# Kernel optimization log

Hardware: AMD Instinct MI355X
Metric: run time of the kernel (lower is better)

## Reference

```python
import jax, jax.numpy as jnp
import numpy as np

N = 50000      # nodes
E = 800000     # edges
IN = 128       # in_feats
HID = 16       # h_feats (per head)
HEADS = 8      # num_heads layer 1
CLS = 40       # num_classes
NEG_SLOPE = 0.2


def setup_inputs() -> dict:
    key = jax.random.key(0)
    ks = jax.random.split(key, 12)
    s = lambda fan: np.float32(1.0 / np.sqrt(fan))
    return {
        "features": jax.random.normal(ks[0], (N, IN), jnp.float32),
        "edge_src": jax.random.randint(ks[1], (E,), 0, N, dtype=jnp.int32),
        "edge_dst": jax.random.randint(ks[2], (E,), 0, N, dtype=jnp.int32),
        # layer 1 params
        "W1": jax.random.normal(ks[3], (IN, HEADS * HID), jnp.float32) * s(IN),
        "al1": jax.random.normal(ks[4], (HEADS, HID), jnp.float32) * s(HID),
        "ar1": jax.random.normal(ks[5], (HEADS, HID), jnp.float32) * s(HID),
        "b1": jnp.zeros((HEADS * HID,), jnp.float32),
        # layer 2 params (1 head)
        "W2": jax.random.normal(ks[6], (HEADS * HID, CLS), jnp.float32) * s(HEADS * HID),
        "al2": jax.random.normal(ks[7], (1, CLS), jnp.float32) * s(CLS),
        "ar2": jax.random.normal(ks[8], (1, CLS), jnp.float32) * s(CLS),
        "b2": jnp.zeros((CLS,), jnp.float32),
    }


def gat_conv(x, W, al, ar, b, src, dst, heads, out_dim):
    # x: [N, F_in] -> feat: [N, H, D]
    feat = (x @ W).reshape(-1, heads, out_dim)
    el = (feat * al).sum(-1)                      # [N, H]
    er = (feat * ar).sum(-1)                      # [N, H]
    e = jax.nn.leaky_relu(el[src] + er[dst], NEG_SLOPE)  # [E, H]
    # segment softmax over destination neighborhoods
    emax = jax.ops.segment_max(e, dst, num_segments=N)   # [N, H]
    emax = jnp.where(jnp.isfinite(emax), emax, jnp.float32(0.0))
    ee = jnp.exp(e - emax[dst])                   # [E, H]
    denom = jax.ops.segment_sum(ee, dst, num_segments=N)
    alpha = ee / (denom[dst] + jnp.float32(1e-9)) # [E, H]
    msg = alpha[:, :, None] * feat[src]           # [E, H, D]
    out = jax.ops.segment_sum(msg, dst, num_segments=N)  # [N, H, D]
    return out + b.reshape(1, heads, out_dim)


def reference(features, edge_src, edge_dst, W1, al1, ar1, b1, W2, al2, ar2, b2):
    h = jax.nn.elu(gat_conv(features, W1, al1, ar1, b1, edge_src, edge_dst, HEADS, HID))
    h = h.reshape(N, HEADS * HID)                 # flatten(1)
    out = gat_conv(h, W2, al2, ar2, b2, edge_src, edge_dst, 1, CLS)
    return out.mean(axis=1)                       # [N, CLS]
```

## Files before the change

### kernel.cpp

```cpp
#include <hip/hip_runtime.h>
#include <hip/hip_bf16.h>

#define N_NODES 50000
#define N_EDGES 800000
#define IN_F    128
#define HID     16
#define HEADS   8
#define F1      128
#define CLS     40
#define CLSP    64
#define NEG     0.2f
#define NEG_INF (-__builtin_inff())
#define SWEEPS      8
#define SWEEP_RANGE 6250
#define STRIDE      96

typedef __bf16 bf16x8 __attribute__((ext_vector_type(8)));
typedef float  f32x4  __attribute__((ext_vector_type(4)));
typedef float  f32x2  __attribute__((ext_vector_type(2)));

__device__ __forceinline__ float leaky(float v) { return v >= 0.0f ? v : NEG * v; }
__device__ __forceinline__ f32x2 unpk(unsigned u) {
    f32x2 r;
    r.x = __uint_as_float(u << 16);
    r.y = __uint_as_float(u & 0xffff0000u);
    return r;
}

__global__ void setup_kernel(const float* __restrict__ W1, const float* __restrict__ W2,
                             __bf16* __restrict__ w1t, __bf16* __restrict__ w2t,
                             int* __restrict__ cursor) {
    int i = blockIdx.x * blockDim.x + threadIdx.x;
    if (i < N_NODES) cursor[i] = 0;
    if (i < 128 * 128) {
        int n = i >> 7, k = i & 127;
        w1t[i] = (__bf16)W1[k * 128 + n];
    }
    if (i < CLSP * 128) {
        int n = i >> 7, k = i & 127;
        w2t[i] = (n < CLS) ? (__bf16)W2[k * CLS + n] : (__bf16)0.0f;
    }
}

__global__ void scatter_kernel(const int* __restrict__ src, const int* __restrict__ dst,
                               int* __restrict__ cursor, int* __restrict__ srcs_sorted) {
    const int BPS = (N_EDGES + 255) / 256;
    int sweep = blockIdx.x / BPS;
    int e = (blockIdx.x - sweep * BPS) * 256 + threadIdx.x;
    if (e >= N_EDGES) return;
    int d = dst[e];
    int lo = sweep * SWEEP_RANGE;
    if (d < lo || d >= lo + SWEEP_RANGE) return;
    int pos = d * STRIDE + atomicAdd(&cursor[d], 1);
    srcs_sorted[pos] = src[e];
}

__global__ __launch_bounds__(256) void gemm1_mfma(const float* __restrict__ A,
                                                  const __bf16* __restrict__ Wt,
                                                  const float* __restrict__ al1,
                                                  const float* __restrict__ ar1,
                                                  __bf16* __restrict__ outb,
                                                  float* __restrict__ el,
                                                  float* __restrict__ er) {
    int wave = threadIdx.x >> 6, lane = threadIdx.x & 63;
    int m0 = blockIdx.x * 64 + wave * 16;
    int c = lane & 15;
    int row = m0 + c;
    int rowc = row < N_NODES ? row : N_NODES - 1;
    int ko = (lane >> 4) * 8;

    f32x4 acc[8];
    #pragma unroll
    for (int t = 0; t < 8; ++t)
        #pragma unroll
        for (int r = 0; r < 4; ++r) acc[t][r] = 0.f;

    for (int ks = 0; ks < 128; ks += 32) {
        const float* ap = A + (size_t)rowc * 128 + ks + ko;
        float4 u = *(const float4*)ap;
        float4 v = *(const float4*)(ap + 4);
        bf16x8 a;
        a[0] = (__bf16)u.x; a[1] = (__bf16)u.y; a[2] = (__bf16)u.z; a[3] = (__bf16)u.w;
        a[4] = (__bf16)v.x; a[5] = (__bf16)v.y; a[6] = (__bf16)v.z; a[7] = (__bf16)v.w;
        #pragma unroll
        for (int t = 0; t < 8; ++t) {
            bf16x8 b = *(const bf16x8*)(Wt + (size_t)(t * 16 + c) * 128 + ks + ko);
            acc[t] = __builtin_amdgcn_mfma_f32_16x16x32_bf16(a, b, acc[t], 0, 0, 0);
        }
    }
    int rbase = m0 + (lane >> 4) * 4;
    #pragma unroll
    for (int t = 0; t < 8; ++t) {
        int gcol = t * 16 + c;
        #pragma unroll
        for (int r = 0; r < 4; ++r) {
            int grow = rbase + r;
            if (grow < N_NODES) outb[(size_t)grow * 128 + gcol] = (__bf16)acc[t][r];
        }
    }
    #pragma unroll
    for (int t = 0; t < 8; ++t) {
        float alv = al1[t * 16 + c];
        float arv = ar1[t * 16 + c];
        float pe[4], pr[4];
        #pragma unroll
        for (int r = 0; r < 4; ++r) { pe[r] = acc[t][r] * alv; pr[r] = acc[t][r] * arv; }
        #pragma unroll
        for (int mask = 1; mask <= 8; mask <<= 1) {
            #pragma unroll
            for (int r = 0; r < 4; ++r) {
                pe[r] += __shfl_xor(pe[r], mask, 64);
                pr[r] += __shfl_xor(pr[r], mask, 64);
            }
        }
        if (c == 0) {
            #pragma unroll
            for (int r = 0; r < 4; ++r) {
                int grow = rbase + r;
                if (grow < N_NODES) {
                    el[grow * 8 + t] = pe[r];
                    er[grow * 8 + t] = pr[r];
                }
            }
        }
    }
}

__global__ __launch_bounds__(256) void gemm2_mfma(const __bf16* __restrict__ A,
                                                  const __bf16* __restrict__ Wt,
                                                  const float* __restrict__ al2,
                                                  const float* __restrict__ ar2,
                                                  __bf16* __restrict__ out,
                                                  float* __restrict__ el,
                                                  float* __restrict__ er) {
    int wave = threadIdx.x >> 6, lane = threadIdx.x & 63;
    int m0 = blockIdx.x * 64 + wave * 16;
    int c = lane & 15;
    int row = m0 + c;
    int rowc = row < N_NODES ? row : N_NODES - 1;
    int ko = (lane >> 4) * 8;

    f32x4 acc[4];
    #pragma unroll
    for (int t = 0; t < 4; ++t)
        #pragma unroll
        for (int r = 0; r < 4; ++r) acc[t][r] = 0.f;

    for (int ks = 0; ks < 128; ks += 32) {
        bf16x8 a = *(const bf16x8*)(A + (size_t)rowc * 128 + ks + ko);
        #pragma unroll
        for (int t = 0; t < 4; ++t) {
            bf16x8 b = *(const bf16x8*)(Wt + (size_t)(t * 16 + c) * 128 + ks + ko);
            acc[t] = __builtin_amdgcn_mfma_f32_16x16x32_bf16(a, b, acc[t], 0, 0, 0);
        }
    }
    int rbase = m0 + (lane >> 4) * 4;
    #pragma unroll
    for (int t = 0; t < 4; ++t) {
        int gcol = t * 16 + c;
        #pragma unroll
        for (int r = 0; r < 4; ++r) {
            int grow = rbase + r;
            if (grow < N_NODES) out[(size_t)grow * CLSP + gcol] = (__bf16)acc[t][r];
        }
    }
    float pe[4] = {0.f, 0.f, 0.f, 0.f}, pr[4] = {0.f, 0.f, 0.f, 0.f};
    #pragma unroll
    for (int t = 0; t < 3; ++t) {
        int idx = t * 16 + c;
        float alv = (idx < CLS) ? al2[idx] : 0.f;
        float arv = (idx < CLS) ? ar2[idx] : 0.f;
        #pragma unroll
        for (int r = 0; r < 4; ++r) { pe[r] += acc[t][r] * alv; pr[r] += acc[t][r] * arv; }
    }
    #pragma unroll
    for (int mask = 1; mask <= 8; mask <<= 1) {
        #pragma unroll
        for (int r = 0; r < 4; ++r) {
            pe[r] += __shfl_xor(pe[r], mask, 64);
            pr[r] += __shfl_xor(pr[r], mask, 64);
        }
    }
    if (c == 0) {
        #pragma unroll
        for (int r = 0; r < 4; ++r) {
            int grow = rbase + r;
            if (grow < N_NODES) { el[grow] = pe[r]; er[grow] = pr[r]; }
        }
    }
}

__global__ __launch_bounds__(256) void gat1_fused(const int* __restrict__ degs,
                                                  const int* __restrict__ srcs,
                                                  const float* __restrict__ el,
                                                  const float* __restrict__ er,
                                                  const __bf16* __restrict__ feat1b,
                                                  const float* __restrict__ b1,
                                                  __bf16* __restrict__ hbufb) {
    __shared__ float a_lds[4][64 * 8];
    __shared__ int   s_lds[4][64];
    int wave = threadIdx.x >> 6;
    int lane = threadIdx.x & 63;
    int d = blockIdx.x * 4 + wave;
    int off = d * STRIDE;
    int deg = degs[d];

    int h = lane & 7, slot = lane >> 3;
    int q = lane >> 4, fg = lane & 15, hd = fg >> 1;
    float er_d = er[d * 8 + h];

    f32x2 accv[4];
    #pragma unroll
    for (int j = 0; j < 4; ++j) { accv[j].x = 0.f; accv[j].y = 0.f; }

    bool fast = (deg <= 64);
    if (fast) {
        int nit = (deg + 7) >> 3;
        float sc[8];
        int sreg[8];
        float m = NEG_INF;
        #pragma unroll
        for (int it = 0; it < 8; ++it) {
            float v = NEG_INF;
            int e = it * 8 + slot;
            if (it < nit && e < deg) {
                sreg[it] = srcs[off + e];
                v = leaky(el[sreg[it] * 8 + h] + er_d);
            }
            sc[it] = v;
            m = fmaxf(m, v);
        }
        float l = 0.f;
        #pragma unroll
        for (int it = 0; it < 8; ++it)
            l += (sc[it] == NEG_INF) ? 0.f : __expf(sc[it] - m);
        #pragma unroll
        for (int mask = 8; mask <= 32; mask <<= 1) {
            float m2 = __shfl_xor(m, mask, 64);
            float l2 = __shfl_xor(l, mask, 64);
            float mn = fmaxf(m, m2);
            float f1 = (m  == NEG_INF) ? 0.f : __expf(m - mn);
            float f2 = (m2 == NEG_INF) ? 0.f : __expf(m2 - mn);
            l = l * f1 + l2 * f2;
            m = mn;
        }
        float inv_l = 1.f / (l + 1e-9f);
        #pragma unroll
        for (int it = 0; it < 8; ++it) {
            int e = it * 8 + slot;
            if (it < nit && e < deg) {
                a_lds[wave][e * 8 + h] = __expf(sc[it] - m) * inv_l;
                if (h == 0) s_lds[wave][e] = sreg[it];
            }
        }
    }
    __syncthreads();

    if (fast) {
        int ng = (deg + 3) >> 2;
        #pragma unroll 4
        for (int g = 0; g < ng; ++g) {
            int k = g * 4 + q;
            float a = 0.f;
            int se = 0;
            if (k < deg) {
                a = a_lds[wave][k * 8 + hd];
                se = s_lds[wave][k];
            }
            uint4 p = *(const uint4*)(feat1b + (size_t)se * F1 + fg * 8);
            f32x2 av; av.x = a; av.y = a;
            accv[0] += av * unpk(p.x);
            accv[1] += av * unpk(p.y);
            accv[2] += av * unpk(p.z);
            accv[3] += av * unpk(p.w);
        }
    } else {
        float m = NEG_INF, l = 0.f;
        for (int base = 0; base < deg; base += 8) {
            int e = base + slot;
            float v = NEG_INF;
            if (e < deg) {
                int s = srcs[off + e];
                v = leaky(el[s * 8 + h] + er_d);
            }
            float mn = fmaxf(m, v);
            float f1 = (m == NEG_INF) ? 0.f : __expf(m - mn);
            float f2 = (v == NEG_INF) ? 0.f : __expf(v - mn);
            l = l * f1 + f2;
            m = mn;
        }
        #pragma unroll
        for (int mask = 8; mask <= 32; mask <<= 1) {
            float m2 = __shfl_xor(m, mask, 64);
            float l2 = __shfl_xor(l, mask, 64);
            float mn = fmaxf(m, m2);
            float f1 = (m  == NEG_INF) ? 0.f : __expf(m - mn);
            float f2 = (m2 == NEG_INF) ? 0.f : __expf(m2 - mn);
            l = l * f1 + l2 * f2;
            m = mn;
        }
        float inv_l = 1.f / (l + 1e-9f);

        for (int base = 0; base < deg; base += 8) {
            int e = base + slot;
            float alpha = 0.f;
            int s = 0;
            if (e < deg) {
                s = srcs[off + e];
                float v = leaky(el[s * 8 + h] + er_d);
                alpha = __expf(v - m) * inv_l;
            }
            #pragma unroll
            for (int sub = 0; sub < 2; ++sub) {
                int k = sub * 4 + q;
                float a  = __shfl(alpha, k * 8 + hd, 64);
                int   se = __shfl(s,     k * 8,      64);
                uint4 p = *(const uint4*)(feat1b + (size_t)se * F1 + fg * 8);
                f32x2 av; av.x = a; av.y = a;
                accv[0] += av * unpk(p.x);
                accv[1] += av * unpk(p.y);
                accv[2] += av * unpk(p.z);
                accv[3] += av * unpk(p.w);
            }
        }
    }

    float acc[8];
    #pragma unroll
    for (int j = 0; j < 4; ++j) { acc[2 * j] = accv[j].x; acc[2 * j + 1] = accv[j].y; }
    #pragma unroll
    for (int i = 0; i < 8; ++i) {
        acc[i] += __shfl_xor(acc[i], 16, 64);
        acc[i] += __shfl_xor(acc[i], 32, 64);
    }
    if (q == 0) {
        bf16x8 o;
        #pragma unroll
        for (int i = 0; i < 8; ++i) {
            float v = acc[i] + b1[fg * 8 + i];
            v = v > 0.f ? v : expm1f(v);
            o[i] = (__bf16)v;
        }
        *(bf16x8*)(hbufb + (size_t)d * F1 + fg * 8) = o;
    }
}

__global__ __launch_bounds__(256) void gat2_fused(const int* __restrict__ degs,
                                                  const int* __restrict__ srcs,
                                                  const float* __restrict__ el,
                                                  const float* __restrict__ er,
                                                  const __bf16* __restrict__ feat2p,
                                                  const float* __restrict__ b2,
                                                  float* __restrict__ out) {
    __shared__ float a_lds[4][64];
    __shared__ int   s_lds[4][64];
    int wave = threadIdx.x >> 6;
    int lane = threadIdx.x & 63;
    int d = blockIdx.x * 4 + wave;
    int off = d * STRIDE;
    int deg = degs[d];

    float er_d = er[d];
    int q  = lane >> 4;
    int cg = lane & 15;
    f32x2 accv[2];
    accv[0].x = 0.f; accv[0].y = 0.f; accv[1].x = 0.f; accv[1].y = 0.f;

    bool fast = (deg <= 64);
    if (fast) {
        float sc = NEG_INF;
        int s0 = 0;
        if (lane < deg) {
            s0 = srcs[off + lane];
            sc = leaky(el[s0] + er_d);
        }
        float m = sc, l = (sc == NEG_INF) ? 0.f : 1.f;
        #pragma unroll
        for (int mask = 1; mask <= 32; mask <<= 1) {
            float m2 = __shfl_xor(m, mask, 64);
            float l2 = __shfl_xor(l, mask, 64);
            float mn = fmaxf(m, m2);
            float f1 = (m  == NEG_INF) ? 0.f : __expf(m - mn);
            float f2 = (m2 == NEG_INF) ? 0.f : __expf(m2 - mn);
            l = l * f1 + l2 * f2;
            m = mn;
        }
        float inv_l = 1.f / (l + 1e-9f);
        if (lane < deg) {
            a_lds[wave][lane] = __expf(sc - m) * inv_l;
            s_lds[wave][lane] = s0;
        }
    }
    __syncthreads();

    if (fast) {
        int ng = (deg + 3) >> 2;
        #pragma unroll 4
        for (int g = 0; g < ng; ++g) {
            int k = g * 4 + q;
            float a = 0.f;
            int se = 0;
            if (k < deg) {
                a = a_lds[wave][k];
                se = s_lds[wave][k];
            }
            uint2 p = *(const uint2*)(feat2p + (size_t)se * CLSP + cg * 4);
            f32x2 av; av.x = a; av.y = a;
            accv[0] += av * unpk(p.x);
            accv[1] += av * unpk(p.y);
        }
    } else {
        float m = NEG_INF, l = 0.f;
        for (int base = 0; base < deg; base += 64) {
            int e = base + lane;
            float sc = NEG_INF;
            if (e < deg) {
                int s = srcs[off + e];
                sc = leaky(el[s] + er_d);
            }
            float mn = fmaxf(m, sc);
            float f1 = (m  == NEG_INF) ? 0.f : __expf(m - mn);
            float f2 = (sc == NEG_INF) ? 0.f : __expf(sc - mn);
            l = l * f1 + f2;
            m = mn;
        }
        #pragma unroll
        for (int mask = 1; mask <= 32; mask <<= 1) {
            float m2 = __shfl_xor(m, mask, 64);
            float l2 = __shfl_xor(l, mask, 64);
            float mn = fmaxf(m, m2);
            float f1 = (m  == NEG_INF) ? 0.f : __expf(m - mn);
            float f2 = (m2 == NEG_INF) ? 0.f : __expf(m2 - mn);
            l = l * f1 + l2 * f2;
            m = mn;
        }
        float inv_l = 1.f / (l + 1e-9f);

        for (int base = 0; base < deg; base += 64) {
            int e = base + lane;
            float alpha = 0.f;
            int s = 0;
            if (e < deg) {
                s = srcs[off + e];
                float sc = leaky(el[s] + er_d);
                alpha = __expf(sc - m) * inv_l;
            }
            int kmax = min(64, deg - base);
            int nsub = (kmax + 3) >> 2;
            for (int sub = 0; sub < nsub; ++sub) {
                int k = sub * 4 + q;
                float a  = __shfl(alpha, k, 64);
                int   se = __shfl(s,     k, 64);
                uint2 p = *(const uint2*)(feat2p + (size_t)se * CLSP + cg * 4);
                f32x2 av; av.x = a; av.y = a;
                accv[0] += av * unpk(p.x);
                accv[1] += av * unpk(p.y);
            }
        }
    }

    float acc[4];
    acc[0] = accv[0].x; acc[1] = accv[0].y; acc[2] = accv[1].x; acc[3] = accv[1].y;
    #pragma unroll
    for (int i = 0; i < 4; ++i) {
        acc[i] += __shfl_xor(acc[i], 16, 64);
        acc[i] += __shfl_xor(acc[i], 32, 64);
    }
    if (lane < 10) {
        float4 o;
        o.x = acc[0] + b2[cg * 4 + 0];
        o.y = acc[1] + b2[cg * 4 + 1];
        o.z = acc[2] + b2[cg * 4 + 2];
        o.w = acc[3] + b2[cg * 4 + 3];
        *(float4*)(out + (size_t)d * CLS + cg * 4) = o;
    }
}

extern "C" void kernel_launch(void* const* d_in, const int* in_sizes, int n_in,
                              void* d_out, int out_size, void* d_ws, size_t ws_size,
                              hipStream_t stream) {
    const float* features = (const float*)d_in[0];
    const int*   esrc     = (const int*)d_in[1];
    const int*   edst     = (const int*)d_in[2];
    const float* W1       = (const float*)d_in[3];
    const float* al1      = (const float*)d_in[4];
    const float* ar1      = (const float*)d_in[5];
    const float* b1       = (const float*)d_in[6];
    const float* W2       = (const float*)d_in[7];
    const float* al2      = (const float*)d_in[8];
    const float* ar2      = (const float*)d_in[9];
    const float* b2       = (const float*)d_in[10];
    float* out = (float*)d_out;

    float* ws = (float*)d_ws;
    float*  el1    = ws;
    float*  er1    = ws + 400000;
    float*  el2    = ws + 800000;
    float*  er2    = ws + 850000;
    int*    cursor = (int*)(ws + 900000);
    int*    srcs   = (int*)(ws + 950000);
    __bf16* feat1b = (__bf16*)(ws + 5750000);
    __bf16* hbufb  = (__bf16*)(ws + 8950000);
    __bf16* feat2p = (__bf16*)(ws + 12150000);
    __bf16* w1t    = (__bf16*)(ws + 13750000);
    __bf16* w2t    = (__bf16*)(ws + 13760000);

    const int B = 256;
    const int BPS = (N_EDGES + 255) / 256;

    setup_kernel<<<(N_NODES + B - 1) / B, B, 0, stream>>>(W1, W2, w1t, w2t, cursor);
    scatter_kernel<<<SWEEPS * BPS, B, 0, stream>>>(esrc, edst, cursor, srcs);

    gemm1_mfma<<<(N_NODES + 63) / 64, 256, 0, stream>>>(features, w1t, al1, ar1,
                                                        feat1b, el1, er1);
    gat1_fused<<<N_NODES / 4, B, 0, stream>>>(cursor, srcs, el1, er1, feat1b, b1, hbufb);

    gemm2_mfma<<<(N_NODES + 63) / 64, 256, 0, stream>>>(hbufb, w2t, al2, ar2,
                                                        feat2p, el2, er2);
    gat2_fused<<<N_NODES / 4, B, 0, stream>>>(cursor, srcs, el2, er2, feat2p, b2, out);
}
```

Before: 269.1 us.

## Prefetch neighbor feature rows into registers before softmax in GAT aggregation

The fast path of both aggregation kernels now issues the gathers of neighbor feature rows into a register array up front, before the attention-score softmax is computed. This lets the feature-load latency overlap with the score and reduction work, and it removes the LDS staging of source indices. To bound register use, the fast path only covers degree up to 32, so nodes with 33–64 neighbors now take the slower two-pass loop. Average degree is 16, so most nodes stay on the fast path, but the extra registers may reduce occupancy.

Measured after the change: 276.9 us. 2.9% more time.

```diff
diff --git a/kernel.cpp b/kernel.cpp
--- a/kernel.cpp
+++ b/kernel.cpp
@@ -197,8 +197,7 @@
                                                   const __bf16* __restrict__ feat1b,
                                                   const float* __restrict__ b1,
                                                   __bf16* __restrict__ hbufb) {
-    __shared__ float a_lds[4][64 * 8];
-    __shared__ int   s_lds[4][64];
+    __shared__ float a_lds[4][32 * 8];
     int wave = threadIdx.x >> 6;
     int lane = threadIdx.x & 63;
     int d = blockIdx.x * 4 + wave;
@@ -213,26 +212,33 @@
     #pragma unroll
     for (int j = 0; j < 4; ++j) { accv[j].x = 0.f; accv[j].y = 0.f; }
 
-    bool fast = (deg <= 64);
+    bool fast = (deg <= 32);
+    uint4 p[8];
     if (fast) {
-        int nit = (deg + 7) >> 3;
-        float sc[8];
-        int sreg[8];
+        #pragma unroll
+        for (int g = 0; g < 8; ++g) {
+            int k = g * 4 + q;
+            if (k < deg) {
+                int se = srcs[off + k];
+                p[g] = *(const uint4*)(feat1b + (size_t)se * F1 + fg * 8);
+            }
+        }
+        float sc[4];
         float m = NEG_INF;
         #pragma unroll
-        for (int it = 0; it < 8; ++it) {
+        for (int it = 0; it < 4; ++it) {
             float v = NEG_INF;
             int e = it * 8 + slot;
-            if (it < nit && e < deg) {
-                sreg[it] = srcs[off + e];
-                v = leaky(el[sreg[it] * 8 + h] + er_d);
+            if (e < deg) {
+                int s = srcs[off + e];
+                v = leaky(el[s * 8 + h] + er_d);
             }
             sc[it] = v;
             m = fmaxf(m, v);
         }
         float l = 0.f;
         #pragma unroll
-        for (int it = 0; it < 8; ++it)
+        for (int it = 0; it < 4; ++it)
             l += (sc[it] == NEG_INF) ? 0.f : __expf(sc[it] - m);
         #pragma unroll
         for (int mask = 8; mask <= 32; mask <<= 1) {
@@ -246,33 +252,26 @@
         }
         float inv_l = 1.f / (l + 1e-9f);
         #pragma unroll
-        for (int it = 0; it < 8; ++it) {
+        for (int it = 0; it < 4; ++it) {
             int e = it * 8 + slot;
-            if (it < nit && e < deg) {
+            if (e < deg)
                 a_lds[wave][e * 8 + h] = __expf(sc[it] - m) * inv_l;
-                if (h == 0) s_lds[wave][e] = sreg[it];
-            }
         }
     }
     __syncthreads();
 
     if (fast) {
-        int ng = (deg + 3) >> 2;
-        #pragma unroll 4
-        for (int g = 0; g < ng; ++g) {
+        #pragma unroll
+        for (int g = 0; g < 8; ++g) {
             int k = g * 4 + q;
-            float a = 0.f;
-            int se = 0;
             if (k < deg) {
-                a = a_lds[wave][k * 8 + hd];
-                se = s_lds[wave][k];
-            }
-            uint4 p = *(const uint4*)(feat1b + (size_t)se * F1 + fg * 8);
-            f32x2 av; av.x = a; av.y = a;
-            accv[0] += av * unpk(p.x);
-            accv[1] += av * unpk(p.y);
-            accv[2] += av * unpk(p.z);
-            accv[3] += av * unpk(p.w);
+                float a = a_lds[wave][k * 8 + hd];
+                f32x2 av; av.x = a; av.y = a;
+                accv[0] += av * unpk(p[g].x);
+                accv[1] += av * unpk(p[g].y);
+                accv[2] += av * unpk(p[g].z);
+                accv[3] += av * unpk(p[g].w);
+            }
         }
     } else {
         float m = NEG_INF, l = 0.f;
@@ -315,12 +314,12 @@
                 int k = sub * 4 + q;
                 float a  = __shfl(alpha, k * 8 + hd, 64);
                 int   se = __shfl(s,     k * 8,      64);
-                uint4 p = *(const uint4*)(feat1b + (size_t)se * F1 + fg * 8);
+                uint4 pp = *(const uint4*)(feat1b + (size_t)se * F1 + fg * 8);
                 f32x2 av; av.x = a; av.y = a;
-                accv[0] += av * unpk(p.x);
-                accv[1] += av * unpk(p.y);
-                accv[2] += av * unpk(p.z);
-                accv[3] += av * unpk(p.w);
+                accv[0] += av * unpk(pp.x);
+                accv[1] += av * unpk(pp.y);
+                accv[2] += av * unpk(pp.z);
+                accv[3] += av * unpk(pp.w);
             }
         }
     }
@@ -352,8 +351,7 @@
                                                   const __bf16* __restrict__ feat2p,
                                                   const float* __restrict__ b2,
                                                   float* __restrict__ out) {
-    __shared__ float a_lds[4][64];
-    __shared__ int   s_lds[4][64];
+    __shared__ float a_lds[4][32];
     int wave = threadIdx.x >> 6;
     int lane = threadIdx.x & 63;
     int d = blockIdx.x * 4 + wave;
@@ -366,12 +364,20 @@
     f32x2 accv[2];
     accv[0].x = 0.f; accv[0].y = 0.f; accv[1].x = 0.f; accv[1].y = 0.f;
 
-    bool fast = (deg <= 64);
+    bool fast = (deg <= 32);
+    uint2 p[8];
     if (fast) {
+        #pragma unroll
+        for (int g = 0; g < 8; ++g) {
+            int k = g * 4 + q;
+            if (k < deg) {
+                int se = srcs[off + k];
+                p[g] = *(const uint2*)(feat2p + (size_t)se * CLSP + cg * 4);
+            }
+        }
         float sc = NEG_INF;
-        int s0 = 0;
         if (lane < deg) {
-            s0 = srcs[off + lane];
+            int s0 = srcs[off + lane];
             sc = leaky(el[s0] + er_d);
         }
         float m = sc, l = (sc == NEG_INF) ? 0.f : 1.f;
@@ -386,28 +392,21 @@
             m = mn;
         }
         float inv_l = 1.f / (l + 1e-9f);
-        if (lane < deg) {
+        if (lane < deg)
             a_lds[wave][lane] = __expf(sc - m) * inv_l;
-            s_lds[wave][lane] = s0;
-        }
     }
     __syncthreads();
 
     if (fast) {
-        int ng = (deg + 3) >> 2;
-        #pragma unroll 4
-        for (int g = 0; g < ng; ++g) {
+        #pragma unroll
+        for (int g = 0; g < 8; ++g) {
             int k = g * 4 + q;
-            float a = 0.f;
-            int se = 0;
             if (k < deg) {
-                a = a_lds[wave][k];
-                se = s_lds[wave][k];
-            }
-            uint2 p = *(const uint2*)(feat2p + (size_t)se * CLSP + cg * 4);
-            f32x2 av; av.x = a; av.y = a;
-            accv[0] += av * unpk(p.x);
-            accv[1] += av * unpk(p.y);
+                float a = a_lds[wave][k];
+                f32x2 av; av.x = a; av.y = a;
+                accv[0] += av * unpk(p[g].x);
+                accv[1] += av * unpk(p[g].y);
+            }
         }
     } else {
         float m = NEG_INF, l = 0.f;
@@ -451,10 +450,10 @@
                 int k = sub * 4 + q;
                 float a  = __shfl(alpha, k, 64);
                 int   se = __shfl(s,     k, 64);
-                uint2 p = *(const uint2*)(feat2p + (size_t)se * CLSP + cg * 4);
+                uint2 pp = *(const uint2*)(feat2p + (size_t)se * CLSP + cg * 4);
                 f32x2 av; av.x = a; av.y = a;
-                accv[0] += av * unpk(p.x);
-                accv[1] += av * unpk(p.y);
+                accv[0] += av * unpk(pp.x);
+                accv[1] += av * unpk(pp.y);
             }
         }
     }
```
